# Optimization experiments

Measured on AMD Instinct MI355X. Metric: run time of the kernel, lower is better.

Reference implementation:

```python
import jax, jax.numpy as jnp
import numpy as np

P = 30000      # nodes (WSI patches)
DIN = 1536     # input feature dim
DOUT = 256     # output dim
HEADS = 2
C = DOUT // HEADS  # per-head channels = 128
E = 320000     # edges (before self-loops)
NEG_SLOPE = 0.2


def setup_inputs() -> dict:
    key = jax.random.key(0)
    ks = jax.random.split(key, 12)
    g = lambda k, shape: jax.random.normal(k, shape, jnp.float32) * 0.02
    return {
        "x": jax.random.normal(ks[0], (P, DIN), jnp.float32),
        "edge_index": jax.random.randint(ks[1], (2, E), 0, P),
        "W1l": g(ks[2], (DIN, DOUT)), "b1l": jnp.zeros((DOUT,), jnp.float32),
        "W1r": g(ks[3], (DIN, DOUT)), "b1r": jnp.zeros((DOUT,), jnp.float32),
        "att1": g(ks[4], (HEADS, C)), "bias1": jnp.zeros((DOUT,), jnp.float32),
        "W2l": g(ks[5], (DOUT, DOUT)), "b2l": jnp.zeros((DOUT,), jnp.float32),
        "W2r": g(ks[6], (DOUT, DOUT)), "b2r": jnp.zeros((DOUT,), jnp.float32),
        "att2": g(ks[7], (HEADS, C)), "bias2": jnp.zeros((DOUT,), jnp.float32),
        "ln1_g": jnp.ones((DOUT,), jnp.float32), "ln1_b": jnp.zeros((DOUT,), jnp.float32),
        "ln2_g": jnp.ones((DOUT,), jnp.float32), "ln2_b": jnp.zeros((DOUT,), jnp.float32),
        "resW": g(ks[8], (DIN, DOUT)), "resb": jnp.zeros((DOUT,), jnp.float32),
    }


def layer_norm(h, g, b, eps=1e-5):
    mu = h.mean(-1, keepdims=True)
    var = ((h - mu) ** 2).mean(-1, keepdims=True)
    return (h - mu) * jax.lax.rsqrt(var + eps) * g + b


def gatv2(x, src, dst, Wl, bl, Wr, br, att, bias):
    # PyG GATv2Conv: lin_l on source j, lin_r on target i,
    # e_ij = att . LeakyReLU(xl[j] + xr[i]); softmax over incoming edges of i;
    # out_i = sum_j alpha_ij * xl[j]  (heads concatenated) + bias.
    n = x.shape[0]
    xl = (x @ Wl + bl).reshape(n, HEADS, C)
    xr = (x @ Wr + br).reshape(n, HEADS, C)
    m = jax.nn.leaky_relu(xl[src] + xr[dst], NEG_SLOPE)      # (Etot, H, C)
    e = jnp.einsum('ehc,hc->eh', m, att)                     # (Etot, H)
    emax = jax.ops.segment_max(e, dst, num_segments=n)       # stable segment softmax
    ex = jnp.exp(e - emax[dst])
    den = jax.ops.segment_sum(ex, dst, num_segments=n)
    alpha = ex / den[dst]                                    # (Etot, H)
    out = jax.ops.segment_sum(xl[src] * alpha[..., None], dst, num_segments=n)
    return out.reshape(n, HEADS * C) + bias


def reference(x, edge_index, W1l, b1l, W1r, b1r, att1, bias1,
              W2l, b2l, W2r, b2r, att2, bias2,
              ln1_g, ln1_b, ln2_g, ln2_b, resW, resb):
    loops = jnp.arange(P)
    src = jnp.concatenate([edge_index[0], loops])  # add self loops
    dst = jnp.concatenate([edge_index[1], loops])

    h1 = gatv2(x, src, dst, W1l, b1l, W1r, b1r, att1, bias1)
    h1 = jax.nn.elu(layer_norm(h1, ln1_g, ln1_b)) + (x @ resW + resb)

    h2 = gatv2(h1, src, dst, W2l, b2l, W2r, b2r, att2, bias2)
    h2 = jax.nn.elu(layer_norm(h2, ln2_g, ln2_b)) + h2 * 0 + h1 + (h2 - h1) * 0 if False else jax.nn.elu(layer_norm(h2, ln2_g, ln2_b)) + h1
    # JK-max combine of the two layer outputs
    return jnp.maximum(h1, h2)
```

## Files before the change

### kernel.cpp

```cpp
#include <hip/hip_runtime.h>
#include <math.h>

#define P_NODES 30000
#define P_PAD   30080
#define DIN_    1536
#define DOUT_   256
#define E_EDGES 320000
#define ET      (E_EDGES + P_NODES)
#define NEG     0.2f

typedef float  f32x4  __attribute__((ext_vector_type(4)));
typedef __bf16 bf16x8 __attribute__((ext_vector_type(8)));
typedef __bf16 bf16x4 __attribute__((ext_vector_type(4)));

__device__ __forceinline__ int swz_col(int c, int row) {
    return (c & ~63) | ((((c >> 3) ^ row) & 7) << 3) | (c & 7);
}

__global__ __launch_bounds__(256)
void cast_x(const float* __restrict__ x, __bf16* __restrict__ XB)
{
    int idx = blockIdx.x * 256 + threadIdx.x;
    if (idx >= P_PAD * 192) return;
    int row = idx / 192;
    int c = (idx - row * 192) * 8;
    int cs = swz_col(c, row);
    bf16x8 o;
    if (row < P_NODES) {
        f32x4 v0 = *(const f32x4*)(x + (size_t)row * DIN_ + c);
        f32x4 v1 = *(const f32x4*)(x + (size_t)row * DIN_ + c + 4);
        #pragma unroll
        for (int j = 0; j < 4; ++j) { o[j] = (__bf16)v0[j]; o[j + 4] = (__bf16)v1[j]; }
    } else {
        #pragma unroll
        for (int j = 0; j < 8; ++j) o[j] = (__bf16)0.f;
    }
    *(bf16x8*)(XB + (size_t)row * DIN_ + cs) = o;
}

__global__ __launch_bounds__(256)
void prep_w1(const float* __restrict__ W1l, const float* __restrict__ W1r,
             const float* __restrict__ resW, __bf16* __restrict__ WT1)
{
    int idx = blockIdx.x * 256 + threadIdx.x;
    if (idx >= DIN_ * 192) return;
    int k = idx / 192;
    int n0 = (idx - k * 192) * 4;
    const float* src; int col;
    if (n0 < 256)      { src = W1l;  col = n0; }
    else if (n0 < 512) { src = W1r;  col = n0 - 256; }
    else               { src = resW; col = n0 - 512; }
    f32x4 v = *(const f32x4*)(src + (size_t)k * DOUT_ + col);
    #pragma unroll
    for (int j = 0; j < 4; ++j) {
        int n = n0 + j;
        WT1[(size_t)n * DIN_ + swz_col(k, n)] = (__bf16)v[j];
    }
}

__global__ __launch_bounds__(256)
void prep_w2(const float* __restrict__ W2l, const float* __restrict__ W2r,
             __bf16* __restrict__ WT2)
{
    int idx = blockIdx.x * 256 + threadIdx.x;
    if (idx >= 256 * 128) return;
    int k = idx / 128;
    int n0 = (idx - k * 128) * 4;
    const float* src; int col;
    if (n0 < 256) { src = W2l; col = n0; }
    else          { src = W2r; col = n0 - 256; }
    f32x4 v = *(const f32x4*)(src + (size_t)k * DOUT_ + col);
    #pragma unroll
    for (int j = 0; j < 4; ++j) {
        int n = n0 + j;
        WT2[(size_t)n * DOUT_ + swz_col(k, n)] = (__bf16)v[j];
    }
}

__global__ void prep_bias(const float* b1l, const float* b1r, const float* resb,
                          const float* b2l, const float* b2r,
                          float* B1, float* B2)
{
    int t = threadIdx.x;
    if (t < 256)      B1[t] = b1l[t];
    else if (t < 512) B1[t] = b1r[t - 256];
    else if (t < 768) B1[t] = resb[t - 512];
    if (t < 256)      B2[t] = b2l[t];
    else if (t < 512) B2[t] = b2r[t - 256];
}

__global__ void init_deg(int* deg)
{
    int i = blockIdx.x * 256 + threadIdx.x;
    if (i < P_NODES) deg[i] = 1;
}

__global__ void hist_kernel(const int* __restrict__ dst, int* __restrict__ deg)
{
    int e = blockIdx.x * 256 + threadIdx.x;
    if (e < E_EDGES) atomicAdd(&deg[dst[e]], 1);
}

__global__ __launch_bounds__(1024)
void scan_kernel(const int* __restrict__ deg, int* __restrict__ offs, int* __restrict__ pos)
{
    __shared__ int sb[1024];
    const int t = threadIdx.x;
    const int base = t * 30;
    int ldv[30];
    int lsum = 0;
    #pragma unroll
    for (int i = 0; i < 30; ++i) {
        int idx = base + i;
        int v = (idx < P_NODES) ? deg[idx] : 0;
        ldv[i] = v; lsum += v;
    }
    sb[t] = lsum; __syncthreads();
    for (int off = 1; off < 1024; off <<= 1) {
        int v = (t >= off) ? sb[t - off] : 0;
        __syncthreads();
        sb[t] += v;
        __syncthreads();
    }
    int excl = sb[t] - lsum;
    #pragma unroll
    for (int i = 0; i < 30; ++i) {
        int idx = base + i;
        if (idx < P_NODES) { offs[idx] = excl; pos[idx] = excl; excl += ldv[i]; }
    }
    if (t == 0) offs[P_NODES] = ET;
}

__global__ void scatter_kernel(const int* __restrict__ ei, int* __restrict__ pos,
                               int* __restrict__ srcs)
{
    int tgt = blockIdx.x * 256 + threadIdx.x;
    if (tgt < E_EDGES) {
        int s = ei[tgt];
        int d = ei[E_EDGES + tgt];
        int p = atomicAdd(&pos[d], 1);
        srcs[p] = s;
    } else if (tgt < ET) {
        int i = tgt - E_EDGES;
        int p = atomicAdd(&pos[i], 1);
        srcs[p] = i;
    }
}

template<int EPI>
__global__ __launch_bounds__(256)
void gemm_kernel(const __bf16* __restrict__ A, const __bf16* __restrict__ WT,
                 const float* __restrict__ bias,
                 __bf16* __restrict__ Cb, float* __restrict__ Cf,
                 int M, int N, int K, int ntiles)
{
    __shared__ __align__(16) __bf16 As[128 * 64];
    __shared__ __align__(16) __bf16 Bs[128 * 64];

    const int bid = blockIdx.x;
    const int mt = bid / ntiles, nt = bid - mt * ntiles;
    const int grow = mt * 128, gcol = nt * 128;
    const int t = threadIdx.x;
    const int lane = t & 63, wave = t >> 6;
    const int wr = wave >> 1, wc = wave & 1;
    const int fr = lane & 15, kg = lane >> 4;
    const int frs = fr & 7;

    const __bf16* agp = A  + (size_t)(grow + (t >> 3)) * K + (t & 7) * 8;
    const __bf16* bgp = WT + (size_t)(gcol + (t >> 3)) * K + (t & 7) * 8;
    const size_t rstep = (size_t)32 * K;
    char* lA = (char*)As + wave * 1024;
    char* lB = (char*)Bs + wave * 1024;

    f32x4 acc[4][4] = {};

    for (int k0 = 0; k0 < K; k0 += 64) {
        __syncthreads();
        #pragma unroll
        for (int i = 0; i < 4; ++i) {
            __builtin_amdgcn_global_load_lds(
                (const __attribute__((address_space(1))) void*)(agp + i * rstep + k0),
                (__attribute__((address_space(3))) void*)(lA + i * 4096), 16, 0, 0);
            __builtin_amdgcn_global_load_lds(
                (const __attribute__((address_space(1))) void*)(bgp + i * rstep + k0),
                (__attribute__((address_space(3))) void*)(lB + i * 4096), 16, 0, 0);
        }
        __syncthreads();

        #pragma unroll
        for (int ks = 0; ks < 2; ++ks) {
            bf16x8 af[4], bv[4];
            #pragma unroll
            for (int mi = 0; mi < 4; ++mi)
                af[mi] = *(const bf16x8*)&As[(wr * 64 + mi * 16 + fr) * 64 + (((ks * 4 + kg) ^ frs)) * 8];
            #pragma unroll
            for (int ni = 0; ni < 4; ++ni)
                bv[ni] = *(const bf16x8*)&Bs[(wc * 64 + ni * 16 + fr) * 64 + (((ks * 4 + kg) ^ frs)) * 8];
            #pragma unroll
            for (int mi = 0; mi < 4; ++mi)
                #pragma unroll
                for (int ni = 0; ni < 4; ++ni)
                    acc[mi][ni] = __builtin_amdgcn_mfma_f32_16x16x32_bf16(af[mi], bv[ni], acc[mi][ni], 0, 0, 0);
        }
    }

    #pragma unroll
    for (int mi = 0; mi < 4; ++mi) {
        #pragma unroll
        for (int ni = 0; ni < 4; ++ni) {
            int col = gcol + wc * 64 + ni * 16 + fr;
            float bvv = bias[col];
            #pragma unroll
            for (int j = 0; j < 4; ++j) {
                int row = grow + wr * 64 + mi * 16 + kg * 4 + j;
                if (row < M) {
                    float v = acc[mi][ni][j] + bvv;
                    if (EPI == 0) {
                        if (col < 512) Cb[(size_t)row * 512 + col] = (__bf16)v;
                        else           Cf[(size_t)row * 256 + col - 512] = v;
                    } else {
                        Cb[(size_t)row * 512 + col] = (__bf16)v;
                    }
                }
            }
        }
    }
}

__global__ __launch_bounds__(256)
void gat_kernel(const __bf16* __restrict__ XLXR,
                const int* __restrict__ offs, const int* __restrict__ srcs,
                const float* __restrict__ att, const float* __restrict__ bias,
                float* __restrict__ out)
{
    const int node = blockIdx.x * 4 + (threadIdx.x >> 6);
    const int lane = threadIdx.x & 63;
    const int c0 = lane * 4;
    bf16x4 xrb = *(const bf16x4*)(XLXR + (size_t)node * 512 + 256 + c0);
    f32x4 xr, at = *(const f32x4*)(att + c0);
    #pragma unroll
    for (int j = 0; j < 4; ++j) xr[j] = (float)xrb[j];
    f32x4 acc = {0.f, 0.f, 0.f, 0.f};
    float m = -INFINITY, den = 0.f;
    const int e1 = offs[node + 1];
    for (int e = offs[node]; e < e1; ++e) {
        int s = srcs[e];
        bf16x4 xlb = *(const bf16x4*)(XLXR + (size_t)s * 512 + c0);
        f32x4 xl;
        float p = 0.f;
        #pragma unroll
        for (int j = 0; j < 4; ++j) {
            xl[j] = (float)xlb[j];
            float tt = xl[j] + xr[j];
            float lr = tt > 0.f ? tt : NEG * tt;
            p = fmaf(at[j], lr, p);
        }
        #pragma unroll
        for (int w = 1; w < 32; w <<= 1) p += __shfl_xor(p, w, 32);
        float nm = fmaxf(m, p);
        float sc = __expf(m - nm);
        float wv = __expf(p - nm);
        den = den * sc + wv;
        #pragma unroll
        for (int j = 0; j < 4; ++j) acc[j] = acc[j] * sc + wv * xl[j];
        m = nm;
    }
    float inv = 1.f / den;
    f32x4 o;
    #pragma unroll
    for (int j = 0; j < 4; ++j) o[j] = acc[j] * inv + bias[c0 + j];
    *(f32x4*)(out + (size_t)node * DOUT_ + c0) = o;
}

__global__ __launch_bounds__(256)
void h1_kernel(const float* __restrict__ GAT, const float* __restrict__ RES,
               const float* __restrict__ g, const float* __restrict__ b,
               float* __restrict__ H1, __bf16* __restrict__ H1B)
{
    const int node = blockIdx.x * 4 + (threadIdx.x >> 6);
    const int lane = threadIdx.x & 63;
    const int c0 = lane * 4;
    const int cs = swz_col(c0, node);
    if (node >= P_NODES) {
        bf16x4 z; 
        #pragma unroll
        for (int j = 0; j < 4; ++j) z[j] = (__bf16)0.f;
        *(bf16x4*)(H1B + (size_t)node * DOUT_ + cs) = z;
        return;
    }
    f32x4 h = *(const f32x4*)(GAT + (size_t)node * DOUT_ + c0);
    float s = h[0] + h[1] + h[2] + h[3];
    #pragma unroll
    for (int w = 1; w < 64; w <<= 1) s += __shfl_xor(s, w, 64);
    float mu = s * (1.f / DOUT_);
    f32x4 d; float sq = 0.f;
    #pragma unroll
    for (int j = 0; j < 4; ++j) { d[j] = h[j] - mu; sq += d[j] * d[j]; }
    #pragma unroll
    for (int w = 1; w < 64; w <<= 1) sq += __shfl_xor(sq, w, 64);
    float rs = rsqrtf(sq * (1.f / DOUT_) + 1e-5f);
    f32x4 res = *(const f32x4*)(RES + (size_t)node * DOUT_ + c0);
    f32x4 o; bf16x4 hb;
    #pragma unroll
    for (int j = 0; j < 4; ++j) {
        float y = d[j] * rs * g[c0 + j] + b[c0 + j];
        float e = y > 0.f ? y : __expf(y) - 1.f;
        o[j] = e + res[j];
        hb[j] = (__bf16)o[j];
    }
    *(f32x4*)(H1 + (size_t)node * DOUT_ + c0) = o;
    *(bf16x4*)(H1B + (size_t)node * DOUT_ + cs) = hb;
}

__global__ __launch_bounds__(256)
void final_kernel(const float* __restrict__ GAT2, const float* __restrict__ H1,
                  const float* __restrict__ g, const float* __restrict__ b,
                  float* __restrict__ out)
{
    const int node = blockIdx.x * 4 + (threadIdx.x >> 6);
    const int lane = threadIdx.x & 63;
    const int c0 = lane * 4;
    f32x4 h = *(const f32x4*)(GAT2 + (size_t)node * DOUT_ + c0);
    float s = h[0] + h[1] + h[2] + h[3];
    #pragma unroll
    for (int w = 1; w < 64; w <<= 1) s += __shfl_xor(s, w, 64);
    float mu = s * (1.f / DOUT_);
    f32x4 d; float sq = 0.f;
    #pragma unroll
    for (int j = 0; j < 4; ++j) { d[j] = h[j] - mu; sq += d[j] * d[j]; }
    #pragma unroll
    for (int w = 1; w < 64; w <<= 1) sq += __shfl_xor(sq, w, 64);
    float rs = rsqrtf(sq * (1.f / DOUT_) + 1e-5f);
    f32x4 h1v = *(const f32x4*)(H1 + (size_t)node * DOUT_ + c0);
    f32x4 o;
    #pragma unroll
    for (int j = 0; j < 4; ++j) {
        float y = d[j] * rs * g[c0 + j] + b[c0 + j];
        float e = y > 0.f ? y : __expf(y) - 1.f;
        float h2 = e + h1v[j];
        o[j] = fmaxf(h1v[j], h2);
    }
    *(f32x4*)(out + (size_t)node * DOUT_ + c0) = o;
}

extern "C" void kernel_launch(void* const* d_in, const int* in_sizes, int n_in,
                              void* d_out, int out_size, void* d_ws, size_t ws_size,
                              hipStream_t stream)
{
    const float* x     = (const float*)d_in[0];
    const int*   ei    = (const int*)d_in[1];
    const float* W1l   = (const float*)d_in[2];
    const float* b1l   = (const float*)d_in[3];
    const float* W1r   = (const float*)d_in[4];
    const float* b1r   = (const float*)d_in[5];
    const float* att1  = (const float*)d_in[6];
    const float* bias1 = (const float*)d_in[7];
    const float* W2l   = (const float*)d_in[8];
    const float* b2l   = (const float*)d_in[9];
    const float* W2r   = (const float*)d_in[10];
    const float* b2r   = (const float*)d_in[11];
    const float* att2  = (const float*)d_in[12];
    const float* bias2 = (const float*)d_in[13];
    const float* ln1g  = (const float*)d_in[14];
    const float* ln1b  = (const float*)d_in[15];
    const float* ln2g  = (const float*)d_in[16];
    const float* ln2b  = (const float*)d_in[17];
    const float* resW  = (const float*)d_in[18];
    const float* resb  = (const float*)d_in[19];
    float* out = (float*)d_out;

    char* w = (char*)d_ws;
    auto alloc = [&](size_t bytes) {
        char* r = w;
        w += (bytes + 255) & ~(size_t)255;
        return r;
    };
    __bf16* XB    = (__bf16*)alloc((size_t)P_PAD * DIN_ * 2);
    __bf16* XLR1  = (__bf16*)alloc((size_t)P_NODES * 512 * 2);
    float*  RES   = (float*)alloc((size_t)P_NODES * 256 * 4);
    float*  H1    = (float*)alloc((size_t)P_NODES * 256 * 4);
    __bf16* WT1   = (__bf16*)alloc((size_t)768 * DIN_ * 2);
    __bf16* WT2   = (__bf16*)alloc((size_t)512 * DOUT_ * 2);
    float*  BIAS1 = (float*)alloc(768 * 4);
    float*  BIAS2 = (float*)alloc(512 * 4);
    int*    deg   = (int*)alloc((size_t)P_NODES * 4);
    int*    offs  = (int*)alloc((size_t)(P_NODES + 1) * 4);
    int*    pos   = (int*)alloc((size_t)(P_NODES + 1) * 4);
    int*    srcs  = (int*)alloc((size_t)ET * 4);

    __bf16* XLR2 = (__bf16*)XB;
    __bf16* H1B  = (__bf16*)((char*)XB + (size_t)32 * 1024 * 1024);
    float*  GAT  = (float*)((char*)XB + (size_t)48 * 1024 * 1024);

    cast_x<<<(P_PAD * 192 + 255) / 256, 256, 0, stream>>>(x, XB);
    prep_w1<<<(DIN_ * 192 + 255) / 256, 256, 0, stream>>>(W1l, W1r, resW, WT1);
    prep_w2<<<(256 * 128 + 255) / 256, 256, 0, stream>>>(W2l, W2r, WT2);
    prep_bias<<<1, 1024, 0, stream>>>(b1l, b1r, resb, b2l, b2r, BIAS1, BIAS2);
    init_deg<<<(P_NODES + 255) / 256, 256, 0, stream>>>(deg);
    hist_kernel<<<(E_EDGES + 255) / 256, 256, 0, stream>>>(ei + E_EDGES, deg);
    scan_kernel<<<1, 1024, 0, stream>>>(deg, offs, pos);
    scatter_kernel<<<(ET + 255) / 256, 256, 0, stream>>>(ei, pos, srcs);

    const int mtiles = P_PAD / 128;

    gemm_kernel<0><<<mtiles * 6, 256, 0, stream>>>(XB, WT1, BIAS1, XLR1, RES, P_NODES, 768, DIN_, 6);
    gat_kernel<<<P_NODES / 4, 256, 0, stream>>>(XLR1, offs, srcs, att1, bias1, GAT);
    h1_kernel<<<P_PAD / 4, 256, 0, stream>>>(GAT, RES, ln1g, ln1b, H1, H1B);

    gemm_kernel<1><<<mtiles * 4, 256, 0, stream>>>(H1B, WT2, BIAS2, XLR2, nullptr, P_NODES, 512, DOUT_, 4);
    gat_kernel<<<P_NODES / 4, 256, 0, stream>>>(XLR2, offs, srcs, att2, bias2, GAT);
    final_kernel<<<P_NODES / 4, 256, 0, stream>>>(GAT, H1, ln2g, ln2b, out);
}
```

Baseline: 659.7 us.

## Fuse GAT aggregation with LayerNorm/ELU epilogue and process 4 edges per wave

Merges the GAT aggregation kernel with the following LayerNorm+ELU+residual (layer 1) and LayerNorm+ELU+JK-max (layer 2) kernels. This drops the fp32 GAT intermediate round-trip and two launches. Each wave now handles four edges at a time: 16-lane groups each hold 8 channels per head, and the groups' partial online-softmax states are merged with shuffles at the end. It also adds an XCD-aware block remapping in the GEMM for better L2 locality, plus a small kernel that zero-fills the padding rows of H1B.

```diff
diff --git a/kernel.cpp b/kernel.cpp
--- a/kernel.cpp
+++ b/kernel.cpp
@@ -8,6 +8,7 @@
 #define E_EDGES 320000
 #define ET      (E_EDGES + P_NODES)
 #define NEG     0.2f
+#define BIG_NEG (-1e30f)
 
 typedef float  f32x4  __attribute__((ext_vector_type(4)));
 typedef __bf16 bf16x8 __attribute__((ext_vector_type(8)));
@@ -15,6 +16,12 @@
 
 __device__ __forceinline__ int swz_col(int c, int row) {
     return (c & ~63) | ((((c >> 3) ^ row) & 7) << 3) | (c & 7);
+}
+
+__device__ __forceinline__ int xcd_swz(int orig, int nwg) {
+    int q = nwg >> 3, r = nwg & 7;
+    int xcd = orig & 7, idx = orig >> 3;
+    return (xcd < r ? xcd * (q + 1) : r * (q + 1) + (xcd - r) * q) + idx;
 }
 
 __global__ __launch_bounds__(256)
@@ -157,7 +164,7 @@
     __shared__ __align__(16) __bf16 As[128 * 64];
     __shared__ __align__(16) __bf16 Bs[128 * 64];
 
-    const int bid = blockIdx.x;
+    const int bid = xcd_swz(blockIdx.x, gridDim.x);
     const int mt = bid / ntiles, nt = bid - mt * ntiles;
     const int grow = mt * 128, gcol = nt * 128;
     const int t = threadIdx.x;
@@ -227,120 +234,175 @@
     }
 }
 
+template<int LAYER>
 __global__ __launch_bounds__(256)
-void gat_kernel(const __bf16* __restrict__ XLXR,
-                const int* __restrict__ offs, const int* __restrict__ srcs,
-                const float* __restrict__ att, const float* __restrict__ bias,
-                float* __restrict__ out)
+void gat_fused(const __bf16* __restrict__ XLXR,
+               const int* __restrict__ offs, const int* __restrict__ srcs,
+               const float* __restrict__ att, const float* __restrict__ bias,
+               const float* __restrict__ lng, const float* __restrict__ lnb,
+               const float* __restrict__ AUX,
+               float* __restrict__ OutF, __bf16* __restrict__ OutB)
 {
     const int node = blockIdx.x * 4 + (threadIdx.x >> 6);
     const int lane = threadIdx.x & 63;
-    const int c0 = lane * 4;
-    bf16x4 xrb = *(const bf16x4*)(XLXR + (size_t)node * 512 + 256 + c0);
-    f32x4 xr, at = *(const f32x4*)(att + c0);
-    #pragma unroll
-    for (int j = 0; j < 4; ++j) xr[j] = (float)xrb[j];
-    f32x4 acc = {0.f, 0.f, 0.f, 0.f};
-    float m = -INFINITY, den = 0.f;
-    const int e1 = offs[node + 1];
-    for (int e = offs[node]; e < e1; ++e) {
-        int s = srcs[e];
-        bf16x4 xlb = *(const bf16x4*)(XLXR + (size_t)s * 512 + c0);
-        f32x4 xl;
-        float p = 0.f;
-        #pragma unroll
-        for (int j = 0; j < 4; ++j) {
-            xl[j] = (float)xlb[j];
-            float tt = xl[j] + xr[j];
+    const int grp = lane >> 4, l = lane & 15;
+    const int ch0 = l * 8, ch1 = 128 + l * 8;
+
+    bf16x8 xr0b = *(const bf16x8*)(XLXR + (size_t)node * 512 + 256 + ch0);
+    bf16x8 xr1b = *(const bf16x8*)(XLXR + (size_t)node * 512 + 256 + ch1);
+    float xr0[8], xr1[8], at0[8], at1[8];
+    #pragma unroll
+    for (int j = 0; j < 8; ++j) { xr0[j] = (float)xr0b[j]; xr1[j] = (float)xr1b[j]; }
+    *(f32x4*)(at0)     = *(const f32x4*)(att + ch0);
+    *(f32x4*)(at0 + 4) = *(const f32x4*)(att + ch0 + 4);
+    *(f32x4*)(at1)     = *(const f32x4*)(att + ch1);
+    *(f32x4*)(at1 + 4) = *(const f32x4*)(att + ch1 + 4);
+
+    float m0 = BIG_NEG, m1 = BIG_NEG, den0 = 0.f, den1 = 0.f;
+    float acc0[8] = {}, acc1[8] = {};
+
+    const int e0 = offs[node], e1 = offs[node + 1];
+    for (int eb = e0; eb < e1; eb += 4) {
+        int e = eb + grp;
+        bool valid = e < e1;
+        int ee = valid ? e : e1 - 1;
+        int s = srcs[ee];
+        const __bf16* xp = XLXR + (size_t)s * 512;
+        bf16x8 a0 = *(const bf16x8*)(xp + ch0);
+        bf16x8 a1 = *(const bf16x8*)(xp + ch1);
+        float xl0[8], xl1[8];
+        float p0 = 0.f, p1 = 0.f;
+        #pragma unroll
+        for (int j = 0; j < 8; ++j) {
+            xl0[j] = (float)a0[j];
+            float tt = xl0[j] + xr0[j];
             float lr = tt > 0.f ? tt : NEG * tt;
-            p = fmaf(at[j], lr, p);
-        }
-        #pragma unroll
-        for (int w = 1; w < 32; w <<= 1) p += __shfl_xor(p, w, 32);
-        float nm = fmaxf(m, p);
-        float sc = __expf(m - nm);
-        float wv = __expf(p - nm);
-        den = den * sc + wv;
-        #pragma unroll
-        for (int j = 0; j < 4; ++j) acc[j] = acc[j] * sc + wv * xl[j];
-        m = nm;
-    }
-    float inv = 1.f / den;
-    f32x4 o;
-    #pragma unroll
-    for (int j = 0; j < 4; ++j) o[j] = acc[j] * inv + bias[c0 + j];
-    *(f32x4*)(out + (size_t)node * DOUT_ + c0) = o;
-}
-
-__global__ __launch_bounds__(256)
-void h1_kernel(const float* __restrict__ GAT, const float* __restrict__ RES,
-               const float* __restrict__ g, const float* __restrict__ b,
-               float* __restrict__ H1, __bf16* __restrict__ H1B)
-{
-    const int node = blockIdx.x * 4 + (threadIdx.x >> 6);
-    const int lane = threadIdx.x & 63;
-    const int c0 = lane * 4;
-    const int cs = swz_col(c0, node);
-    if (node >= P_NODES) {
-        bf16x4 z; 
-        #pragma unroll
-        for (int j = 0; j < 4; ++j) z[j] = (__bf16)0.f;
-        *(bf16x4*)(H1B + (size_t)node * DOUT_ + cs) = z;
-        return;
-    }
-    f32x4 h = *(const f32x4*)(GAT + (size_t)node * DOUT_ + c0);
-    float s = h[0] + h[1] + h[2] + h[3];
-    #pragma unroll
-    for (int w = 1; w < 64; w <<= 1) s += __shfl_xor(s, w, 64);
-    float mu = s * (1.f / DOUT_);
-    f32x4 d; float sq = 0.f;
-    #pragma unroll
-    for (int j = 0; j < 4; ++j) { d[j] = h[j] - mu; sq += d[j] * d[j]; }
-    #pragma unroll
-    for (int w = 1; w < 64; w <<= 1) sq += __shfl_xor(sq, w, 64);
-    float rs = rsqrtf(sq * (1.f / DOUT_) + 1e-5f);
-    f32x4 res = *(const f32x4*)(RES + (size_t)node * DOUT_ + c0);
-    f32x4 o; bf16x4 hb;
-    #pragma unroll
-    for (int j = 0; j < 4; ++j) {
-        float y = d[j] * rs * g[c0 + j] + b[c0 + j];
-        float e = y > 0.f ? y : __expf(y) - 1.f;
-        o[j] = e + res[j];
-        hb[j] = (__bf16)o[j];
-    }
-    *(f32x4*)(H1 + (size_t)node * DOUT_ + c0) = o;
-    *(bf16x4*)(H1B + (size_t)node * DOUT_ + cs) = hb;
-}
-
-__global__ __launch_bounds__(256)
-void final_kernel(const float* __restrict__ GAT2, const float* __restrict__ H1,
-                  const float* __restrict__ g, const float* __restrict__ b,
-                  float* __restrict__ out)
-{
-    const int node = blockIdx.x * 4 + (threadIdx.x >> 6);
-    const int lane = threadIdx.x & 63;
-    const int c0 = lane * 4;
-    f32x4 h = *(const f32x4*)(GAT2 + (size_t)node * DOUT_ + c0);
-    float s = h[0] + h[1] + h[2] + h[3];
-    #pragma unroll
-    for (int w = 1; w < 64; w <<= 1) s += __shfl_xor(s, w, 64);
-    float mu = s * (1.f / DOUT_);
-    f32x4 d; float sq = 0.f;
-    #pragma unroll
-    for (int j = 0; j < 4; ++j) { d[j] = h[j] - mu; sq += d[j] * d[j]; }
-    #pragma unroll
-    for (int w = 1; w < 64; w <<= 1) sq += __shfl_xor(sq, w, 64);
-    float rs = rsqrtf(sq * (1.f / DOUT_) + 1e-5f);
-    f32x4 h1v = *(const f32x4*)(H1 + (size_t)node * DOUT_ + c0);
-    f32x4 o;
-    #pragma unroll
-    for (int j = 0; j < 4; ++j) {
-        float y = d[j] * rs * g[c0 + j] + b[c0 + j];
-        float e = y > 0.f ? y : __expf(y) - 1.f;
-        float h2 = e + h1v[j];
-        o[j] = fmaxf(h1v[j], h2);
-    }
-    *(f32x4*)(out + (size_t)node * DOUT_ + c0) = o;
+            p0 = fmaf(at0[j], lr, p0);
+            xl1[j] = (float)a1[j];
+            float t1 = xl1[j] + xr1[j];
+            float l1 = t1 > 0.f ? t1 : NEG * t1;
+            p1 = fmaf(at1[j], l1, p1);
+        }
+        #pragma unroll
+        for (int w = 1; w < 16; w <<= 1) {
+            p0 += __shfl_xor(p0, w);
+            p1 += __shfl_xor(p1, w);
+        }
+        if (!valid) { p0 = BIG_NEG; p1 = BIG_NEG; }
+        float nm0 = fmaxf(m0, p0), nm1 = fmaxf(m1, p1);
+        float sc0 = __expf(m0 - nm0), wv0 = __expf(p0 - nm0);
+        float sc1 = __expf(m1 - nm1), wv1 = __expf(p1 - nm1);
+        den0 = den0 * sc0 + wv0;
+        den1 = den1 * sc1 + wv1;
+        #pragma unroll
+        for (int j = 0; j < 8; ++j) {
+            acc0[j] = acc0[j] * sc0 + wv0 * xl0[j];
+            acc1[j] = acc1[j] * sc1 + wv1 * xl1[j];
+        }
+        m0 = nm0; m1 = nm1;
+    }
+
+    #pragma unroll
+    for (int w = 16; w <= 32; w <<= 1) {
+        float mb0 = __shfl_xor(m0, w), db0 = __shfl_xor(den0, w);
+        float mb1 = __shfl_xor(m1, w), db1 = __shfl_xor(den1, w);
+        float M0 = fmaxf(m0, mb0), M1 = fmaxf(m1, mb1);
+        float sa0 = __expf(m0 - M0), sb0 = __expf(mb0 - M0);
+        float sa1 = __expf(m1 - M1), sb1 = __expf(mb1 - M1);
+        den0 = den0 * sa0 + db0 * sb0;
+        den1 = den1 * sa1 + db1 * sb1;
+        #pragma unroll
+        for (int j = 0; j < 8; ++j) {
+            float ab0 = __shfl_xor(acc0[j], w);
+            float ab1 = __shfl_xor(acc1[j], w);
+            acc0[j] = acc0[j] * sa0 + ab0 * sb0;
+            acc1[j] = acc1[j] * sa1 + ab1 * sb1;
+        }
+        m0 = M0; m1 = M1;
+    }
+
+    float inv0 = 1.f / den0, inv1 = 1.f / den1;
+    float o0[8], o1[8];
+    #pragma unroll
+    for (int j = 0; j < 8; ++j) {
+        o0[j] = acc0[j] * inv0 + bias[ch0 + j];
+        o1[j] = acc1[j] * inv1 + bias[ch1 + j];
+    }
+
+    float s = 0.f;
+    #pragma unroll
+    for (int j = 0; j < 8; ++j) s += o0[j] + o1[j];
+    #pragma unroll
+    for (int w = 1; w < 16; w <<= 1) s += __shfl_xor(s, w);
+    float mu = s * (1.f / 256.f);
+    float sq = 0.f;
+    #pragma unroll
+    for (int j = 0; j < 8; ++j) {
+        o0[j] -= mu; o1[j] -= mu;
+        sq += o0[j] * o0[j] + o1[j] * o1[j];
+    }
+    #pragma unroll
+    for (int w = 1; w < 16; w <<= 1) sq += __shfl_xor(sq, w);
+    float rs = rsqrtf(sq * (1.f / 256.f) + 1e-5f);
+
+    float g0[8], g1[8], bb0[8], bb1[8], x0[8], x1[8];
+    *(f32x4*)(g0)      = *(const f32x4*)(lng + ch0);
+    *(f32x4*)(g0 + 4)  = *(const f32x4*)(lng + ch0 + 4);
+    *(f32x4*)(g1)      = *(const f32x4*)(lng + ch1);
+    *(f32x4*)(g1 + 4)  = *(const f32x4*)(lng + ch1 + 4);
+    *(f32x4*)(bb0)     = *(const f32x4*)(lnb + ch0);
+    *(f32x4*)(bb0 + 4) = *(const f32x4*)(lnb + ch0 + 4);
+    *(f32x4*)(bb1)     = *(const f32x4*)(lnb + ch1);
+    *(f32x4*)(bb1 + 4) = *(const f32x4*)(lnb + ch1 + 4);
+    *(f32x4*)(x0)      = *(const f32x4*)(AUX + (size_t)node * 256 + ch0);
+    *(f32x4*)(x0 + 4)  = *(const f32x4*)(AUX + (size_t)node * 256 + ch0 + 4);
+    *(f32x4*)(x1)      = *(const f32x4*)(AUX + (size_t)node * 256 + ch1);
+    *(f32x4*)(x1 + 4)  = *(const f32x4*)(AUX + (size_t)node * 256 + ch1 + 4);
+
+    float r0[8], r1[8];
+    #pragma unroll
+    for (int j = 0; j < 8; ++j) {
+        float y0 = o0[j] * rs * g0[j] + bb0[j];
+        float y1 = o1[j] * rs * g1[j] + bb1[j];
+        float e0v = y0 > 0.f ? y0 : __expf(y0) - 1.f;
+        float e1v = y1 > 0.f ? y1 : __expf(y1) - 1.f;
+        if (LAYER == 1) {
+            r0[j] = e0v + x0[j];
+            r1[j] = e1v + x1[j];
+        } else {
+            float h20 = e0v + x0[j];
+            float h21 = e1v + x1[j];
+            r0[j] = fmaxf(x0[j], h20);
+            r1[j] = fmaxf(x1[j], h21);
+        }
+    }
+
+    if (grp == 0) {
+        float* op = OutF + (size_t)node * 256;
+        *(f32x4*)(op + ch0)     = *(f32x4*)(r0);
+        *(f32x4*)(op + ch0 + 4) = *(f32x4*)(r0 + 4);
+        *(f32x4*)(op + ch1)     = *(f32x4*)(r1);
+        *(f32x4*)(op + ch1 + 4) = *(f32x4*)(r1 + 4);
+        if (LAYER == 1) {
+            bf16x8 hb0, hb1;
+            #pragma unroll
+            for (int j = 0; j < 8; ++j) { hb0[j] = (__bf16)r0[j]; hb1[j] = (__bf16)r1[j]; }
+            *(bf16x8*)(OutB + (size_t)node * 256 + swz_col(ch0, node)) = hb0;
+            *(bf16x8*)(OutB + (size_t)node * 256 + swz_col(ch1, node)) = hb1;
+        }
+    }
+}
+
+__global__ void pad_h1b(__bf16* __restrict__ H1B)
+{
+    int i = blockIdx.x * 256 + threadIdx.x;
+    if (i >= (P_PAD - P_NODES) * 32) return;
+    int row = P_NODES + (i >> 5);
+    int c = (i & 31) * 8;
+    bf16x8 z;
+    #pragma unroll
+    for (int j = 0; j < 8; ++j) z[j] = (__bf16)0.f;
+    *(bf16x8*)(H1B + (size_t)row * 256 + c) = z;
 }
 
 extern "C" void kernel_launch(void* const* d_in, const int* in_sizes, int n_in,
@@ -390,7 +452,6 @@
 
     __bf16* XLR2 = (__bf16*)XB;
     __bf16* H1B  = (__bf16*)((char*)XB + (size_t)32 * 1024 * 1024);
-    float*  GAT  = (float*)((char*)XB + (size_t)48 * 1024 * 1024);
 
     cast_x<<<(P_PAD * 192 + 255) / 256, 256, 0, stream>>>(x, XB);
     prep_w1<<<(DIN_ * 192 + 255) / 256, 256, 0, stream>>>(W1l, W1r, resW, WT1);
@@ -404,10 +465,11 @@
     const int mtiles = P_PAD / 128;
 
     gemm_kernel<0><<<mtiles * 6, 256, 0, stream>>>(XB, WT1, BIAS1, XLR1, RES, P_NODES, 768, DIN_, 6);
-    gat_kernel<<<P_NODES / 4, 256, 0, stream>>>(XLR1, offs, srcs, att1, bias1, GAT);
-    h1_kernel<<<P_PAD / 4, 256, 0, stream>>>(GAT, RES, ln1g, ln1b, H1, H1B);
+    gat_fused<1><<<P_NODES / 4, 256, 0, stream>>>(XLR1, offs, srcs, att1, bias1,
+                                                  ln1g, ln1b, RES, H1, H1B);
+    pad_h1b<<<((P_PAD - P_NODES) * 32 + 255) / 256, 256, 0, stream>>>(H1B);
 
     gemm_kernel<1><<<mtiles * 4, 256, 0, stream>>>(H1B, WT2, BIAS2, XLR2, nullptr, P_NODES, 512, DOUT_, 4);
-    gat_kernel<<<P_NODES / 4, 256, 0, stream>>>(XLR2, offs, srcs, att2, bias2, GAT);
-    final_kernel<<<P_NODES / 4, 256, 0, stream>>>(GAT, H1, ln2g, ln2b, out);
-}
+    gat_fused<2><<<P_NODES / 4, 256, 0, stream>>>(XLR2, offs, srcs, att2, bias2,
+                                                  ln2g, ln2b, H1, out, nullptr);
+}
```

Result: no change. 653.6 us (-0.9%).
